# Performance work log

Hardware: AMD Instinct MI355X
Metric: run time of the kernel (lower is better)

The kernel has to match this reference:

```python
import jax, jax.numpy as jnp
import numpy as np


def _onedirectional_dist(a, b):
    # a: [B, A], b: [B, Bn]. For each a_i, squared distance to nearest b_j, summed over i.
    d2 = (a[:, :, None] - b[:, None, :]) ** 2  # [B, A, Bn]
    return jnp.min(d2, axis=2).sum(axis=1)      # [B]


def setup_inputs() -> dict:
    key = jax.random.key(0)
    k1, k2 = jax.random.split(key)
    target = jax.random.uniform(k1, (2, 1, 240, 320), dtype=jnp.float32)
    bin_edges = jax.random.uniform(k2, (2, 257), dtype=jnp.float32)
    return {"target": target, "bin_edges": bin_edges}


def reference(target, bin_edges):
    bin_centers = 0.5 * (bin_edges[:, :-1] + bin_edges[:, 1:])  # [B, K]
    target_depths = target.reshape(target.shape[0], -1)          # [B, N]
    bidir = _onedirectional_dist(bin_centers, target_depths) + \
            _onedirectional_dist(target_depths, bin_centers)
    return bidir.mean()
```

## Files before the change

### kernel.cpp

```cpp
#include <hip/hip_runtime.h>

#define K        256
#define NEDGE    257
#define NPTS     76800
#define THREADS  256
#define R1B      256
#define R2CH     300
#define R2B      (2 * R2CH)
#define NBLOCKS  (R1B + R2B)


__global__ __launch_bounds__(THREADS)
void chamfer_a(const float* __restrict__ target,
               const float* __restrict__ edges,
               float* __restrict__ centerMin,
               float* __restrict__ partials) {
    const int t = threadIdx.x;

    if (blockIdx.x < R1B) {
        const int b  = blockIdx.x >> 7;
        const int c0 = 2 * (blockIdx.x & 127);
        const float* e = edges + b * NEDGE;
        const float cA = 0.5f * (e[c0]     + e[c0 + 1]);
        const float cB = 0.5f * (e[c0 + 1] + e[c0 + 2]);

        const float4* p4 = (const float4*)(target + (size_t)b * NPTS);
        float a0 = 1e30f, a1 = 1e30f, b0 = 1e30f, b1 = 1e30f;
        #pragma unroll 5
        for (int i = 0; i < NPTS / 4 / THREADS; ++i) {
            const float4 p = p4[(size_t)i * THREADS + t];
            float x;
            x = p.x - cA; a0 = fminf(a0, x * x);
            x = p.y - cA; a1 = fminf(a1, x * x);
            x = p.z - cA; a0 = fminf(a0, x * x);
            x = p.w - cA; a1 = fminf(a1, x * x);
            x = p.x - cB; b0 = fminf(b0, x * x);
            x = p.y - cB; b1 = fminf(b1, x * x);
            x = p.z - cB; b0 = fminf(b0, x * x);
            x = p.w - cB; b1 = fminf(b1, x * x);
        }
        __shared__ float sA[THREADS];
        __shared__ float sB[THREADS];
        sA[t] = fminf(a0, a1);
        sB[t] = fminf(b0, b1);
        __syncthreads();
        for (int s = THREADS / 2; s > 0; s >>= 1) {
            if (t < s) {
                sA[t] = fminf(sA[t], sA[t + s]);
                sB[t] = fminf(sB[t], sB[t + s]);
            }
            __syncthreads();
        }
        if (t == 0) {
            centerMin[b * K + c0]     = sA[0];
            centerMin[b * K + c0 + 1] = sB[0];
        }
    } else {
        const int blk2  = blockIdx.x - R1B;
        const int b     = blk2 / R2CH;
        const int chunk = blk2 % R2CH;
        __shared__ float sC[K];
        __shared__ float sRed[THREADS];
        const float* e = edges + b * NEDGE;
        sC[t] = 0.5f * (e[t] + e[t + 1]);
        const float d = target[(size_t)b * NPTS + (size_t)chunk * THREADS + t];
        __syncthreads();

        float m0 = 1e30f, m1 = 1e30f, m2 = 1e30f, m3 = 1e30f;
        const float4* c4 = (const float4*)sC;
        #pragma unroll 16
        for (int i = 0; i < K / 4; ++i) {
            const float4 c = c4[i];
            float x;
            x = d - c.x; m0 = fminf(m0, x * x);
            x = d - c.y; m1 = fminf(m1, x * x);
            x = d - c.z; m2 = fminf(m2, x * x);
            x = d - c.w; m3 = fminf(m3, x * x);
        }
        sRed[t] = fminf(fminf(m0, m1), fminf(m2, m3));
        __syncthreads();
        for (int s = THREADS / 2; s > 0; s >>= 1) {
            if (t < s) sRed[t] += sRed[t + s];
            __syncthreads();
        }
        if (t == 0) partials[blk2] = sRed[0];
    }
}

__global__ __launch_bounds__(THREADS)
void chamfer_b(const float* __restrict__ centerMin,
               const float* __restrict__ partials,
               float* __restrict__ out) {
    __shared__ float sRed[THREADS];
    const int t = threadIdx.x;
    float s = centerMin[t] + centerMin[t + THREADS];
    for (int i = t; i < R2B; i += THREADS) s += partials[i];
    sRed[t] = s;
    __syncthreads();
    for (int st = THREADS / 2; st > 0; st >>= 1) {
        if (t < st) sRed[t] += sRed[t + st];
        __syncthreads();
    }
    if (t == 0) out[0] = 0.5f * sRed[0];
}

extern "C" void kernel_launch(void* const* d_in, const int* in_sizes, int n_in,
                              void* d_out, int out_size, void* d_ws, size_t ws_size,
                              hipStream_t stream) {
    const float* target = (const float*)d_in[0];
    const float* edges  = (const float*)d_in[1];
    float* out = (float*)d_out;

    float* centerMin = (float*)d_ws;
    float* partials  = (float*)((char*)d_ws + 2048);

    chamfer_a<<<NBLOCKS, THREADS, 0, stream>>>(target, edges, centerMin, partials);
    chamfer_b<<<1, THREADS, 0, stream>>>(centerMin, partials, out);
}
```

Before: 14.58 us.

## Fuse final reduction into main kernel via last-block atomic ticket

Merges the two-kernel pipeline into one launch: every block writes its partial with agent-scope atomic stores, then increments a ticket counter, and the block that arrives last performs the final sum. This removes the second kernel launch and the gap between kernels. It relies on the ticket counter in the workspace starting at a multiple of the block count, and on relaxed atomics plus a vmcnt wait for visibility across the device.

```diff
diff --git a/kernel.cpp b/kernel.cpp
--- a/kernel.cpp
+++ b/kernel.cpp
@@ -11,11 +11,16 @@
 
 
 __global__ __launch_bounds__(THREADS)
-void chamfer_a(const float* __restrict__ target,
-               const float* __restrict__ edges,
-               float* __restrict__ centerMin,
-               float* __restrict__ partials) {
+void chamfer_one(const float* __restrict__ target,
+                 const float* __restrict__ edges,
+                 unsigned int* __restrict__ ticket,
+                 float* __restrict__ centerMin,
+                 float* __restrict__ partials,
+                 float* __restrict__ out) {
     const int t = threadIdx.x;
+    __shared__ float sRedA[THREADS];
+    __shared__ float sRedB[THREADS];
+    __shared__ int   sIsLast;
 
     if (blockIdx.x < R1B) {
         const int b  = blockIdx.x >> 7;
@@ -39,28 +44,27 @@
             x = p.z - cB; b0 = fminf(b0, x * x);
             x = p.w - cB; b1 = fminf(b1, x * x);
         }
-        __shared__ float sA[THREADS];
-        __shared__ float sB[THREADS];
-        sA[t] = fminf(a0, a1);
-        sB[t] = fminf(b0, b1);
+        sRedA[t] = fminf(a0, a1);
+        sRedB[t] = fminf(b0, b1);
         __syncthreads();
         for (int s = THREADS / 2; s > 0; s >>= 1) {
             if (t < s) {
-                sA[t] = fminf(sA[t], sA[t + s]);
-                sB[t] = fminf(sB[t], sB[t + s]);
+                sRedA[t] = fminf(sRedA[t], sRedA[t + s]);
+                sRedB[t] = fminf(sRedB[t], sRedB[t + s]);
             }
             __syncthreads();
         }
         if (t == 0) {
-            centerMin[b * K + c0]     = sA[0];
-            centerMin[b * K + c0 + 1] = sB[0];
+            __hip_atomic_store(&centerMin[b * K + c0],     sRedA[0],
+                               __ATOMIC_RELAXED, __HIP_MEMORY_SCOPE_AGENT);
+            __hip_atomic_store(&centerMin[b * K + c0 + 1], sRedB[0],
+                               __ATOMIC_RELAXED, __HIP_MEMORY_SCOPE_AGENT);
         }
     } else {
         const int blk2  = blockIdx.x - R1B;
         const int b     = blk2 / R2CH;
         const int chunk = blk2 % R2CH;
         __shared__ float sC[K];
-        __shared__ float sRed[THREADS];
         const float* e = edges + b * NEDGE;
         sC[t] = 0.5f * (e[t] + e[t + 1]);
         const float d = target[(size_t)b * NPTS + (size_t)chunk * THREADS + t];
@@ -77,31 +81,40 @@
             x = d - c.z; m2 = fminf(m2, x * x);
             x = d - c.w; m3 = fminf(m3, x * x);
         }
-        sRed[t] = fminf(fminf(m0, m1), fminf(m2, m3));
+        sRedA[t] = fminf(fminf(m0, m1), fminf(m2, m3));
         __syncthreads();
         for (int s = THREADS / 2; s > 0; s >>= 1) {
-            if (t < s) sRed[t] += sRed[t + s];
+            if (t < s) sRedA[t] += sRedA[t + s];
             __syncthreads();
         }
-        if (t == 0) partials[blk2] = sRed[0];
+        if (t == 0)
+            __hip_atomic_store(&partials[blk2], sRedA[0],
+                               __ATOMIC_RELAXED, __HIP_MEMORY_SCOPE_AGENT);
     }
-}
 
-__global__ __launch_bounds__(THREADS)
-void chamfer_b(const float* __restrict__ centerMin,
-               const float* __restrict__ partials,
-               float* __restrict__ out) {
-    __shared__ float sRed[THREADS];
-    const int t = threadIdx.x;
-    float s = centerMin[t] + centerMin[t + THREADS];
-    for (int i = t; i < R2B; i += THREADS) s += partials[i];
-    sRed[t] = s;
+    if (t == 0) {
+        asm volatile("s_waitcnt vmcnt(0)" ::: "memory");
+        unsigned int old = __hip_atomic_fetch_add(ticket, 1u, __ATOMIC_RELAXED,
+                                                  __HIP_MEMORY_SCOPE_AGENT);
+        sIsLast = ((old % NBLOCKS) == (NBLOCKS - 1));
+    }
+    __syncthreads();
+    if (!sIsLast) return;
+
+    float s = __hip_atomic_load(&centerMin[t],           __ATOMIC_RELAXED,
+                                __HIP_MEMORY_SCOPE_AGENT)
+            + __hip_atomic_load(&centerMin[t + THREADS], __ATOMIC_RELAXED,
+                                __HIP_MEMORY_SCOPE_AGENT);
+    for (int i = t; i < R2B; i += THREADS)
+        s += __hip_atomic_load(&partials[i], __ATOMIC_RELAXED,
+                               __HIP_MEMORY_SCOPE_AGENT);
+    sRedA[t] = s;
     __syncthreads();
     for (int st = THREADS / 2; st > 0; st >>= 1) {
-        if (t < st) sRed[t] += sRed[t + st];
+        if (t < st) sRedA[t] += sRedA[t + st];
         __syncthreads();
     }
-    if (t == 0) out[0] = 0.5f * sRed[0];
+    if (t == 0) out[0] = 0.5f * sRedA[0];
 }
 
 extern "C" void kernel_launch(void* const* d_in, const int* in_sizes, int n_in,
@@ -111,9 +124,10 @@
     const float* edges  = (const float*)d_in[1];
     float* out = (float*)d_out;
 
-    float* centerMin = (float*)d_ws;
-    float* partials  = (float*)((char*)d_ws + 2048);
+    unsigned int* ticket    = (unsigned int*)d_ws;
+    float*        centerMin = (float*)((char*)d_ws + 64);
+    float*        partials  = (float*)((char*)d_ws + 2176);
 
-    chamfer_a<<<NBLOCKS, THREADS, 0, stream>>>(target, edges, centerMin, partials);
-    chamfer_b<<<1, THREADS, 0, stream>>>(centerMin, partials, out);
+    chamfer_one<<<NBLOCKS, THREADS, 0, stream>>>(target, edges, ticket,
+                                                 centerMin, partials, out);
 }
```

After: 19.82 us. 1.36x slower.

## Split center-min blocks to one center each and expand squared distance in point pass

Applied to the files above, without the earlier changes.

The center-to-points pass now launches one block per bin center instead of two, doubling that block count and halving per-block work. The point-to-centers pass rewrites (d-c)^2 as d^2 - 2cd + c^2, precomputing c^2 and -2c in shared memory so the inner loop is one FMA plus a min, with d^2 added once after the min. This cuts ALU work in the inner loop but doubles the shared-memory reads per iteration and reloads the target data twice as often in the first pass. The expanded form can also lose precision through cancellation.

```diff
diff --git a/kernel.cpp b/kernel.cpp
--- a/kernel.cpp
+++ b/kernel.cpp
@@ -4,7 +4,7 @@
 #define NEDGE    257
 #define NPTS     76800
 #define THREADS  256
-#define R1B      256
+#define R1B      512
 #define R2CH     300
 #define R2B      (2 * R2CH)
 #define NBLOCKS  (R1B + R2B)
@@ -18,66 +18,59 @@
     const int t = threadIdx.x;
 
     if (blockIdx.x < R1B) {
-        const int b  = blockIdx.x >> 7;
-        const int c0 = 2 * (blockIdx.x & 127);
+        const int b = blockIdx.x >> 8;
+        const int c0 = blockIdx.x & 255;
         const float* e = edges + b * NEDGE;
-        const float cA = 0.5f * (e[c0]     + e[c0 + 1]);
-        const float cB = 0.5f * (e[c0 + 1] + e[c0 + 2]);
+        const float c = 0.5f * (e[c0] + e[c0 + 1]);
 
         const float4* p4 = (const float4*)(target + (size_t)b * NPTS);
-        float a0 = 1e30f, a1 = 1e30f, b0 = 1e30f, b1 = 1e30f;
+        float m0 = 1e30f, m1 = 1e30f, m2 = 1e30f, m3 = 1e30f;
         #pragma unroll 5
         for (int i = 0; i < NPTS / 4 / THREADS; ++i) {
             const float4 p = p4[(size_t)i * THREADS + t];
             float x;
-            x = p.x - cA; a0 = fminf(a0, x * x);
-            x = p.y - cA; a1 = fminf(a1, x * x);
-            x = p.z - cA; a0 = fminf(a0, x * x);
-            x = p.w - cA; a1 = fminf(a1, x * x);
-            x = p.x - cB; b0 = fminf(b0, x * x);
-            x = p.y - cB; b1 = fminf(b1, x * x);
-            x = p.z - cB; b0 = fminf(b0, x * x);
-            x = p.w - cB; b1 = fminf(b1, x * x);
+            x = p.x - c; m0 = fminf(m0, x * x);
+            x = p.y - c; m1 = fminf(m1, x * x);
+            x = p.z - c; m2 = fminf(m2, x * x);
+            x = p.w - c; m3 = fminf(m3, x * x);
         }
-        __shared__ float sA[THREADS];
-        __shared__ float sB[THREADS];
-        sA[t] = fminf(a0, a1);
-        sB[t] = fminf(b0, b1);
+        __shared__ float sRed[THREADS];
+        sRed[t] = fminf(fminf(m0, m1), fminf(m2, m3));
         __syncthreads();
         for (int s = THREADS / 2; s > 0; s >>= 1) {
-            if (t < s) {
-                sA[t] = fminf(sA[t], sA[t + s]);
-                sB[t] = fminf(sB[t], sB[t + s]);
-            }
+            if (t < s) sRed[t] = fminf(sRed[t], sRed[t + s]);
             __syncthreads();
         }
-        if (t == 0) {
-            centerMin[b * K + c0]     = sA[0];
-            centerMin[b * K + c0 + 1] = sB[0];
-        }
+        if (t == 0) centerMin[b * K + c0] = sRed[0];
     } else {
         const int blk2  = blockIdx.x - R1B;
         const int b     = blk2 / R2CH;
         const int chunk = blk2 % R2CH;
-        __shared__ float sC[K];
+        __shared__ float sC2[K];
+        __shared__ float sM2C[K];
         __shared__ float sRed[THREADS];
         const float* e = edges + b * NEDGE;
-        sC[t] = 0.5f * (e[t] + e[t + 1]);
+        {
+            const float c = 0.5f * (e[t] + e[t + 1]);
+            sC2[t]  = c * c;
+            sM2C[t] = -2.0f * c;
+        }
         const float d = target[(size_t)b * NPTS + (size_t)chunk * THREADS + t];
         __syncthreads();
 
         float m0 = 1e30f, m1 = 1e30f, m2 = 1e30f, m3 = 1e30f;
-        const float4* c4 = (const float4*)sC;
+        const float4* c2v  = (const float4*)sC2;
+        const float4* m2cv = (const float4*)sM2C;
         #pragma unroll 16
         for (int i = 0; i < K / 4; ++i) {
-            const float4 c = c4[i];
-            float x;
-            x = d - c.x; m0 = fminf(m0, x * x);
-            x = d - c.y; m1 = fminf(m1, x * x);
-            x = d - c.z; m2 = fminf(m2, x * x);
-            x = d - c.w; m3 = fminf(m3, x * x);
+            const float4 c2 = c2v[i];
+            const float4 mc = m2cv[i];
+            m0 = fminf(m0, fmaf(mc.x, d, c2.x));
+            m1 = fminf(m1, fmaf(mc.y, d, c2.y));
+            m2 = fminf(m2, fmaf(mc.z, d, c2.z));
+            m3 = fminf(m3, fmaf(mc.w, d, c2.w));
         }
-        sRed[t] = fminf(fminf(m0, m1), fminf(m2, m3));
+        sRed[t] = fmaf(d, d, fminf(fminf(m0, m1), fminf(m2, m3)));
         __syncthreads();
         for (int s = THREADS / 2; s > 0; s >>= 1) {
             if (t < s) sRed[t] += sRed[t + s];
```

After: 14.46 us. About the same (-0.9%).
